# Performance work log

Hardware: AMD Instinct MI355X
Metric: run time of the kernel (lower is better)

Reference implementation:

```python
import jax, jax.numpy as jnp
import numpy as np

N, E, G = 20000, 600000, 128
NF, HID, L, H = 16, 128, 4, 4
C = HID // H  # 32 per-head out dim
BN_EPS = 1e-5


def setup_inputs() -> dict:
    key = jax.random.key(0)
    ks = jax.random.split(key, 24)
    inp = {}
    inp['x'] = jax.random.normal(ks[0], (N, NF), dtype=jnp.float32)
    inp['edge_index'] = jax.random.randint(ks[1], (2, E), 0, N, dtype=jnp.int32)
    inp['batch'] = jnp.sort(jax.random.randint(ks[2], (N,), 0, G, dtype=jnp.int32))
    s = 0.05
    inp['emb_w'] = jax.random.normal(ks[3], (NF, HID), dtype=jnp.float32) * s
    inp['emb_b'] = jnp.zeros((HID,), dtype=jnp.float32)
    inp['gat_w'] = jax.random.normal(ks[4], (L, HID, HID), dtype=jnp.float32) * s
    inp['att_src'] = jax.random.normal(ks[5], (L, H, C), dtype=jnp.float32) * s
    inp['att_dst'] = jax.random.normal(ks[6], (L, H, C), dtype=jnp.float32) * s
    inp['gat_b'] = jnp.zeros((L, HID), dtype=jnp.float32)
    inp['bn_gamma'] = jnp.ones((L, HID), dtype=jnp.float32)
    inp['bn_beta'] = jnp.zeros((L, HID), dtype=jnp.float32)
    inp['bn_mean'] = jax.random.normal(ks[7], (L, HID), dtype=jnp.float32) * 0.01
    inp['bn_var'] = jnp.ones((L, HID), dtype=jnp.float32)
    inp['fc1_w'] = jax.random.normal(ks[8], (HID, 64), dtype=jnp.float32) * s
    inp['fc1_b'] = jnp.zeros((64,), dtype=jnp.float32)
    inp['fc2_w'] = jax.random.normal(ks[9], (64, 32), dtype=jnp.float32) * s
    inp['fc2_b'] = jnp.zeros((32,), dtype=jnp.float32)
    inp['bg_w'] = jax.random.normal(ks[10], (32, 1), dtype=jnp.float32) * s
    inp['bg_b'] = jnp.zeros((1,), dtype=jnp.float32)
    return inp


def _gat_layer(x, W, a_src, a_dst, bias, src, dst):
    # PyG GATConv (concat=True, negative_slope=0.2, self-loops already appended)
    h = (x @ W).reshape(N, H, C)                      # [N,H,C]
    s_src = jnp.sum(h * a_src, axis=-1)               # [N,H]
    s_dst = jnp.sum(h * a_dst, axis=-1)               # [N,H]
    e = jax.nn.leaky_relu(s_src[src] + s_dst[dst], 0.2)  # [E+N,H]
    m = jax.ops.segment_max(e, dst, num_segments=N)   # per-dest softmax max
    ex = jnp.exp(e - m[dst])
    denom = jax.ops.segment_sum(ex, dst, num_segments=N)
    alpha = ex / (denom[dst] + 1e-16)                 # [E+N,H]
    msg = h[src] * alpha[:, :, None]                  # [E+N,H,C]
    out = jax.ops.segment_sum(msg, dst, num_segments=N)
    return out.reshape(N, HID) + bias


def reference(x, edge_index, batch, emb_w, emb_b, gat_w, att_src, att_dst, gat_b,
              bn_gamma, bn_beta, bn_mean, bn_var, fc1_w, fc1_b, fc2_w, fc2_b, bg_w, bg_b):
    # add self loops (PyG GATConv default)
    loops = jnp.arange(N, dtype=edge_index.dtype)
    src = jnp.concatenate([edge_index[0], loops])
    dst = jnp.concatenate([edge_index[1], loops])

    h = jax.nn.relu(x @ emb_w + emb_b)
    for l in range(L):
        hn = _gat_layer(h, gat_w[l], att_src[l], att_dst[l], gat_b[l], src, dst)
        hn = (hn - bn_mean[l]) * (bn_gamma[l] / jnp.sqrt(bn_var[l] + BN_EPS)) + bn_beta[l]
        h = h + jax.nn.relu(hn)

    # global mean pool over graphs
    sums = jax.ops.segment_sum(h, batch, num_segments=G)
    cnts = jax.ops.segment_sum(jnp.ones((N,), dtype=h.dtype), batch, num_segments=G)
    g = sums / jnp.maximum(cnts, 1.0)[:, None]        # [G,HID]

    g = jax.nn.relu(g @ fc1_w + fc1_b)
    g = jax.nn.relu(g @ fc2_w + fc2_b)
    out = g @ bg_w + bg_b                              # band_gap head
    return out.squeeze(-1)                             # [G]
```

## Files before the change

kernel.cpp:

```cpp
#include <hip/hip_runtime.h>
#include <math.h>

#define HID 128
#define NF  16
#define NH  4
#define HC  32
#define NLAYERS 4
#define SCAN_B 256

__global__ void k_init(int* __restrict__ counts, int N,
                       const float* __restrict__ gat_b, const float* __restrict__ gamma,
                       const float* __restrict__ beta, const float* __restrict__ mean,
                       const float* __restrict__ var,
                       float* __restrict__ scale, float* __restrict__ shift) {
    int i = blockIdx.x * blockDim.x + threadIdx.x;
    if (i < N) counts[i] = 1;
    if (i < NLAYERS * HID) {
        float sc = gamma[i] / sqrtf(var[i] + 1e-5f);
        scale[i] = sc;
        shift[i] = beta[i] + (gat_b[i] - mean[i]) * sc;
    }
}

__global__ void k_count_edges(const int* __restrict__ dst, int E, int* __restrict__ counts) {
    int i = blockIdx.x * blockDim.x + threadIdx.x;
    if (i < E) atomicAdd(&counts[dst[i]], 1);
}

__global__ __launch_bounds__(SCAN_B) void k_partial(const int* __restrict__ counts,
                                                    int* __restrict__ partials, int N) {
    __shared__ int s[SCAN_B];
    const int t = threadIdx.x;
    const int i = blockIdx.x * SCAN_B + t;
    int v = (i < N) ? counts[i] : 0;
    s[t] = v;
    __syncthreads();
#pragma unroll
    for (int off = SCAN_B / 2; off >= 1; off >>= 1) {
        if (t < off) s[t] += s[t + off];
        __syncthreads();
    }
    if (t == 0) partials[blockIdx.x] = s[0];
}

__global__ __launch_bounds__(128) void k_scanp(const int* __restrict__ partials,
                                               int* __restrict__ bases,
                                               int* __restrict__ row_ptr_N, int B) {
    __shared__ int s[128];
    const int t = threadIdx.x;
    int v = (t < B) ? partials[t] : 0;
    s[t] = v;
    __syncthreads();
    for (int off = 1; off < 128; off <<= 1) {
        int u = (t >= off) ? s[t - off] : 0;
        __syncthreads();
        s[t] += u;
        __syncthreads();
    }
    if (t < B) bases[t] = s[t] - v;
    if (t == 127) *row_ptr_N = s[127];
}

__global__ __launch_bounds__(SCAN_B) void k_final(const int* __restrict__ counts,
                                                  const int* __restrict__ bases,
                                                  int* __restrict__ row_ptr,
                                                  int* __restrict__ col,
                                                  int* __restrict__ fill, int N) {
    __shared__ int s[SCAN_B];
    const int t = threadIdx.x;
    const int i = blockIdx.x * SCAN_B + t;
    const int v = (i < N) ? counts[i] : 0;
    s[t] = v;
    __syncthreads();
    for (int off = 1; off < SCAN_B; off <<= 1) {
        int u = (t >= off) ? s[t - off] : 0;
        __syncthreads();
        s[t] += u;
        __syncthreads();
    }
    if (i < N) {
        const int row = bases[blockIdx.x] + s[t] - v;
        row_ptr[i] = row;
        col[row] = i;
        fill[i] = 1;
    }
}

__global__ void k_scatter(const int* __restrict__ src, const int* __restrict__ dst, int E,
                          const int* __restrict__ row_ptr, int* __restrict__ fill,
                          int* __restrict__ col) {
    int i = blockIdx.x * blockDim.x + threadIdx.x;
    if (i < E) {
        int d = dst[i];
        int pos = atomicAdd(&fill[d], 1);
        col[row_ptr[d] + pos] = src[i];
    }
}

__global__ __launch_bounds__(256) void k_embed(const float* __restrict__ x,
                                               const float* __restrict__ w,
                                               const float* __restrict__ b,
                                               float* __restrict__ h, int N) {
    __shared__ float ws_[NF * HID];
    __shared__ float bs[HID];
    const int t = threadIdx.x;
    for (int i = t; i < NF * HID; i += 256) ws_[i] = w[i];
    if (t < HID) bs[t] = b[t];
    __syncthreads();
    const int n = blockIdx.x * 2 + (t >> 7);
    const int j = t & 127;
    if (n >= N) return;
    float a = bs[j];
    const float4* xp = (const float4*)(x + (size_t)n * NF);
#pragma unroll
    for (int q = 0; q < 4; ++q) {
        const float4 xv = xp[q];
        a = fmaf(xv.x, ws_[(q * 4 + 0) * HID + j], a);
        a = fmaf(xv.y, ws_[(q * 4 + 1) * HID + j], a);
        a = fmaf(xv.z, ws_[(q * 4 + 2) * HID + j], a);
        a = fmaf(xv.w, ws_[(q * 4 + 3) * HID + j], a);
    }
    h[(size_t)n * HID + j] = fmaxf(a, 0.f);
}

__global__ __launch_bounds__(256) void k_gemm_attn(
    const float* __restrict__ h, const float* __restrict__ W,
    const float* __restrict__ a_src, const float* __restrict__ a_dst,
    float* __restrict__ hproj, float* __restrict__ ssrc, float* __restrict__ sdst, int N) {
    __shared__ float As[2][16][68];
    __shared__ float Bs[2][16][132];
    const int tid = threadIdx.x;
    const int m0 = blockIdx.x * 64;
    const int tx = tid & 15;
    const int ty = tid >> 4;
    float acc[4][8];
#pragma unroll
    for (int i = 0; i < 4; ++i)
#pragma unroll
        for (int j = 0; j < 8; ++j) acc[i][j] = 0.f;

    const int arow = tid >> 2;
    const int ak   = (tid & 3) << 2;
    const int brow = tid >> 4;
    const int bcol = (tid & 15) << 3;
    const int gr = m0 + arow;
    const float* aptr = h + (size_t)gr * HID + ak;
    const float* bptr = W + brow * HID + bcol;

    float4 av = (gr < N) ? *(const float4*)aptr : make_float4(0.f, 0.f, 0.f, 0.f);
    float4 bv0 = *(const float4*)bptr;
    float4 bv1 = *(const float4*)(bptr + 4);
    As[0][ak + 0][arow] = av.x; As[0][ak + 1][arow] = av.y;
    As[0][ak + 2][arow] = av.z; As[0][ak + 3][arow] = av.w;
    *(float4*)&Bs[0][brow][bcol] = bv0;
    *(float4*)&Bs[0][brow][bcol + 4] = bv1;
    __syncthreads();

    for (int k0 = 0; k0 < 8; ++k0) {
        const int cur = k0 & 1, nxt = cur ^ 1;
        if (k0 < 7) {
            av = (gr < N) ? *(const float4*)(aptr + (k0 + 1) * 16)
                          : make_float4(0.f, 0.f, 0.f, 0.f);
            bv0 = *(const float4*)(bptr + (size_t)(k0 + 1) * 16 * HID);
            bv1 = *(const float4*)(bptr + (size_t)(k0 + 1) * 16 * HID + 4);
        }
#pragma unroll
        for (int k = 0; k < 16; ++k) {
            const float4 a  = *(const float4*)&As[cur][k][ty << 2];
            const float4 b0 = *(const float4*)&Bs[cur][k][tx << 3];
            const float4 b1 = *(const float4*)&Bs[cur][k][(tx << 3) + 4];
            const float aa[4] = {a.x, a.y, a.z, a.w};
            const float bb[8] = {b0.x, b0.y, b0.z, b0.w, b1.x, b1.y, b1.z, b1.w};
#pragma unroll
            for (int i = 0; i < 4; ++i)
#pragma unroll
                for (int j = 0; j < 8; ++j) acc[i][j] = fmaf(aa[i], bb[j], acc[i][j]);
        }
        if (k0 < 7) {
            As[nxt][ak + 0][arow] = av.x; As[nxt][ak + 1][arow] = av.y;
            As[nxt][ak + 2][arow] = av.z; As[nxt][ak + 3][arow] = av.w;
            *(float4*)&Bs[nxt][brow][bcol] = bv0;
            *(float4*)&Bs[nxt][brow][bcol + 4] = bv1;
        }
        __syncthreads();
    }

    const int head = tx >> 2;
    float asv[8], adv[8];
#pragma unroll
    for (int j = 0; j < 8; ++j) {
        asv[j] = a_src[head * HC + (tx & 3) * 8 + j];
        adv[j] = a_dst[head * HC + (tx & 3) * 8 + j];
    }
#pragma unroll
    for (int i = 0; i < 4; ++i) {
        const int r = m0 + (ty << 2) + i;
        if (r < N) {
            const float4 o0 = make_float4(acc[i][0], acc[i][1], acc[i][2], acc[i][3]);
            const float4 o1 = make_float4(acc[i][4], acc[i][5], acc[i][6], acc[i][7]);
            *(float4*)(hproj + (size_t)r * HID + (tx << 3)) = o0;
            *(float4*)(hproj + (size_t)r * HID + (tx << 3) + 4) = o1;
            float ps = 0.f, pd = 0.f;
#pragma unroll
            for (int j = 0; j < 8; ++j) {
                ps = fmaf(acc[i][j], asv[j], ps);
                pd = fmaf(acc[i][j], adv[j], pd);
            }
            ps += __shfl_xor(ps, 1); ps += __shfl_xor(ps, 2);
            pd += __shfl_xor(pd, 1); pd += __shfl_xor(pd, 2);
            if ((tx & 3) == 0) { ssrc[r * NH + head] = ps; sdst[r * NH + head] = pd; }
        }
    }
}

#define LEAKY(e) ((e) > 0.f ? (e) : 0.2f * (e))
__global__ __launch_bounds__(256) void k_sagg(
    float* __restrict__ h, const float4* __restrict__ hproj4,
    const float4* __restrict__ ssrc4, const float4* __restrict__ sdst4,
    const int* __restrict__ row_ptr, const int* __restrict__ col,
    const float4* __restrict__ scale4, const float4* __restrict__ shift4, int N) {
    __shared__ int   s_col[4][64];
    __shared__ float s_alpha[4][256];
    const int t = threadIdx.x;
    const int w = t >> 6;
    const int lane = t & 63;
    const int n = blockIdx.x * 4 + w;
    if (n >= N) return;
    const int beg = row_ptr[n], end = row_ptr[n + 1];
    const float4 sd = sdst4[n];

    const int i0 = beg + lane;
    const bool v0 = i0 < end;
    int sn0 = 0;
    float fe0 = -1e30f, fe1 = -1e30f, fe2 = -1e30f, fe3 = -1e30f;
    float M0 = -1e30f, M1 = -1e30f, M2 = -1e30f, M3 = -1e30f;
    if (v0) {
        sn0 = col[i0];
        const float4 ss = ssrc4[sn0];
        fe0 = LEAKY(ss.x + sd.x); fe1 = LEAKY(ss.y + sd.y);
        fe2 = LEAKY(ss.z + sd.z); fe3 = LEAKY(ss.w + sd.w);
        M0 = fe0; M1 = fe1; M2 = fe2; M3 = fe3;
    }
    for (int i = i0 + 64; i < end; i += 64) {
        const float4 ss = ssrc4[col[i]];
        M0 = fmaxf(M0, LEAKY(ss.x + sd.x));
        M1 = fmaxf(M1, LEAKY(ss.y + sd.y));
        M2 = fmaxf(M2, LEAKY(ss.z + sd.z));
        M3 = fmaxf(M3, LEAKY(ss.w + sd.w));
    }
#pragma unroll
    for (int o = 32; o >= 1; o >>= 1) {
        M0 = fmaxf(M0, __shfl_xor(M0, o));
        M1 = fmaxf(M1, __shfl_xor(M1, o));
        M2 = fmaxf(M2, __shfl_xor(M2, o));
        M3 = fmaxf(M3, __shfl_xor(M3, o));
    }
    float S0 = 0.f, S1 = 0.f, S2 = 0.f, S3 = 0.f;
    float t0 = 0.f, t1 = 0.f, t2 = 0.f, t3 = 0.f;
    if (v0) {
        t0 = __expf(fe0 - M0); t1 = __expf(fe1 - M1);
        t2 = __expf(fe2 - M2); t3 = __expf(fe3 - M3);
        S0 = t0; S1 = t1; S2 = t2; S3 = t3;
    }
    for (int i = i0 + 64; i < end; i += 64) {
        const float4 ss = ssrc4[col[i]];
        S0 += __expf(LEAKY(ss.x + sd.x) - M0);
        S1 += __expf(LEAKY(ss.y + sd.y) - M1);
        S2 += __expf(LEAKY(ss.z + sd.z) - M2);
        S3 += __expf(LEAKY(ss.w + sd.w) - M3);
    }
#pragma unroll
    for (int o = 32; o >= 1; o >>= 1) {
        S0 += __shfl_xor(S0, o);
        S1 += __shfl_xor(S1, o);
        S2 += __shfl_xor(S2, o);
        S3 += __shfl_xor(S3, o);
    }
    const float inv0 = 1.f / (S0 + 1e-16f);
    const float inv1 = 1.f / (S1 + 1e-16f);
    const float inv2 = 1.f / (S2 + 1e-16f);
    const float inv3 = 1.f / (S3 + 1e-16f);

    const int c  = lane & 31;
    const int hh = c >> 3;
    const int eh = lane >> 5;
    float4 acc = make_float4(0.f, 0.f, 0.f, 0.f);
    {
        if (v0) {
            s_col[w][lane] = sn0;
            float4 a;
            a.x = t0 * inv0; a.y = t1 * inv1; a.z = t2 * inv2; a.w = t3 * inv3;
            *(float4*)&s_alpha[w][lane << 2] = a;
        }
        asm volatile("s_waitcnt lgkmcnt(0)" ::: "memory");
        const int cnt = min(64, end - beg);
#pragma unroll 4
        for (int j2 = 0; j2 < cnt; j2 += 2) {
            const int j = j2 + eh;
            float a = 0.f; int sn = s_col[w][0];
            if (j < cnt) { sn = s_col[w][j]; a = s_alpha[w][(j << 2) | hh]; }
            const float4 hv = hproj4[(size_t)sn * 32 + c];
            acc.x = fmaf(a, hv.x, acc.x);
            acc.y = fmaf(a, hv.y, acc.y);
            acc.z = fmaf(a, hv.z, acc.z);
            acc.w = fmaf(a, hv.w, acc.w);
        }
    }
    for (int c0 = beg + 64; c0 < end; c0 += 64) {
        const int i = c0 + lane;
        if (i < end) {
            const int sn = col[i];
            const float4 ss = ssrc4[sn];
            float4 a;
            a.x = __expf(LEAKY(ss.x + sd.x) - M0) * inv0;
            a.y = __expf(LEAKY(ss.y + sd.y) - M1) * inv1;
            a.z = __expf(LEAKY(ss.z + sd.z) - M2) * inv2;
            a.w = __expf(LEAKY(ss.w + sd.w) - M3) * inv3;
            s_col[w][lane] = sn;
            *(float4*)&s_alpha[w][lane << 2] = a;
        }
        asm volatile("s_waitcnt lgkmcnt(0)" ::: "memory");
        const int cnt = min(64, end - c0);
#pragma unroll 4
        for (int j2 = 0; j2 < cnt; j2 += 2) {
            const int j = j2 + eh;
            float a = 0.f; int sn = s_col[w][0];
            if (j < cnt) { sn = s_col[w][j]; a = s_alpha[w][(j << 2) | hh]; }
            const float4 hv = hproj4[(size_t)sn * 32 + c];
            acc.x = fmaf(a, hv.x, acc.x);
            acc.y = fmaf(a, hv.y, acc.y);
            acc.z = fmaf(a, hv.z, acc.z);
            acc.w = fmaf(a, hv.w, acc.w);
        }
    }
    acc.x += __shfl_xor(acc.x, 32);
    acc.y += __shfl_xor(acc.y, 32);
    acc.z += __shfl_xor(acc.z, 32);
    acc.w += __shfl_xor(acc.w, 32);

    if (lane < 32) {
        const float4 sc = scale4[c];
        const float4 sh = shift4[c];
        float4* hp = (float4*)h + (size_t)n * 32 + c;
        float4 hv = *hp;
        hv.x += fmaxf(fmaf(acc.x, sc.x, sh.x), 0.f);
        hv.y += fmaxf(fmaf(acc.y, sc.y, sh.y), 0.f);
        hv.z += fmaxf(fmaf(acc.z, sc.z, sh.z), 0.f);
        hv.w += fmaxf(fmaf(acc.w, sc.w, sh.w), 0.f);
        *hp = hv;
    }
}

__global__ __launch_bounds__(256) void k_poolhead(
    const float4* __restrict__ h4, const int* __restrict__ batch,
    const float* __restrict__ w1, const float* __restrict__ b1,
    const float* __restrict__ w2, const float* __restrict__ b2,
    const float* __restrict__ w3, const float* __restrict__ b3,
    float* __restrict__ out, int N) {
    __shared__ float4 red[8][32];
    __shared__ float gp[HID];
    __shared__ float l1[64];
    __shared__ float l2[32];
    const int g = blockIdx.x;
    const int t = threadIdx.x;
    const int c4 = t & 31, r = t >> 5;
    int lo = 0, hi = N;
    while (lo < hi) { int mid = (lo + hi) >> 1; if (batch[mid] < g) lo = mid + 1; else hi = mid; }
    int lo2 = lo, hi2 = N;
    while (lo2 < hi2) { int mid = (lo2 + hi2) >> 1; if (batch[mid] < g + 1) lo2 = mid + 1; else hi2 = mid; }
    float4 acc = make_float4(0.f, 0.f, 0.f, 0.f);
    for (int i = lo + r; i < lo2; i += 8) {
        const float4 v = h4[(size_t)i * 32 + c4];
        acc.x += v.x; acc.y += v.y; acc.z += v.z; acc.w += v.w;
    }
    red[r][c4] = acc;
    __syncthreads();
    if (r == 0) {
#pragma unroll
        for (int k = 1; k < 8; ++k) {
            const float4 v = red[k][c4];
            acc.x += v.x; acc.y += v.y; acc.z += v.z; acc.w += v.w;
        }
        const float invc = 1.f / fmaxf((float)(lo2 - lo), 1.f);
        float4 o = make_float4(acc.x * invc, acc.y * invc, acc.z * invc, acc.w * invc);
        *(float4*)&gp[c4 << 2] = o;
    }
    __syncthreads();
    if (t < 64) {
        float a = b1[t];
        for (int k = 0; k < HID; ++k) a = fmaf(gp[k], w1[k * 64 + t], a);
        l1[t] = fmaxf(a, 0.f);
    }
    __syncthreads();
    if (t < 32) {
        float a2 = b2[t];
        for (int k = 0; k < 64; ++k) a2 = fmaf(l1[k], w2[k * 32 + t], a2);
        l2[t] = fmaxf(a2, 0.f);
    }
    __syncthreads();
    if (t == 0) {
        float a3 = b3[0];
        for (int k = 0; k < 32; ++k) a3 = fmaf(l2[k], w3[k], a3);
        out[g] = a3;
    }
}

extern "C" void kernel_launch(void* const* d_in, const int* in_sizes, int n_in,
                              void* d_out, int out_size, void* d_ws, size_t ws_size,
                              hipStream_t stream) {
    const float* x        = (const float*)d_in[0];
    const int*   eidx     = (const int*)d_in[1];
    const int*   batch    = (const int*)d_in[2];
    const float* emb_w    = (const float*)d_in[3];
    const float* emb_b    = (const float*)d_in[4];
    const float* gat_w    = (const float*)d_in[5];
    const float* att_src  = (const float*)d_in[6];
    const float* att_dst  = (const float*)d_in[7];
    const float* gat_b    = (const float*)d_in[8];
    const float* bn_gamma = (const float*)d_in[9];
    const float* bn_beta  = (const float*)d_in[10];
    const float* bn_mean  = (const float*)d_in[11];
    const float* bn_var   = (const float*)d_in[12];
    const float* fc1_w    = (const float*)d_in[13];
    const float* fc1_b    = (const float*)d_in[14];
    const float* fc2_w    = (const float*)d_in[15];
    const float* fc2_b    = (const float*)d_in[16];
    const float* bg_w     = (const float*)d_in[17];
    const float* bg_b     = (const float*)d_in[18];
    float* out = (float*)d_out;

    const int N = in_sizes[0] / NF;
    const int E = in_sizes[1] / 2;
    const int G = out_size;

    const int* esrc = eidx;
    const int* edst = eidx + E;

    char* ws = (char*)d_ws;
    size_t off = 0;
    auto alloc = [&](size_t bytes) -> void* {
        void* p = ws + off;
        off += (bytes + 255) & ~(size_t)255;
        return p;
    };
    float*  h        = (float*)alloc((size_t)N * HID * sizeof(float));
    float*  hproj    = (float*)alloc((size_t)N * HID * sizeof(float));
    float*  ssrc     = (float*)alloc((size_t)N * NH * sizeof(float));
    float*  sdst     = (float*)alloc((size_t)N * NH * sizeof(float));
    float*  bnscale  = (float*)alloc((size_t)NLAYERS * HID * sizeof(float));
    float*  bnshift  = (float*)alloc((size_t)NLAYERS * HID * sizeof(float));
    int*    row_ptr  = (int*)alloc((size_t)(N + 1) * sizeof(int));
    int*    counts   = (int*)alloc((size_t)N * sizeof(int));
    int*    col      = (int*)alloc((size_t)(E + N) * sizeof(int));
    int*    partials = (int*)alloc(1024 * sizeof(int));
    int*    bases    = (int*)alloc(1024 * sizeof(int));
    (void)ws_size; (void)n_in;

    const int TB = 256;
    const int NB = (N + SCAN_B - 1) / SCAN_B;

    k_init<<<(N + TB - 1) / TB, TB, 0, stream>>>(counts, N, gat_b, bn_gamma, bn_beta,
                                                 bn_mean, bn_var, bnscale, bnshift);
    k_count_edges<<<(E + TB - 1) / TB, TB, 0, stream>>>(edst, E, counts);
    k_partial<<<NB, SCAN_B, 0, stream>>>(counts, partials, N);
    k_scanp<<<1, 128, 0, stream>>>(partials, bases, row_ptr + N, NB);
    k_final<<<NB, SCAN_B, 0, stream>>>(counts, bases, row_ptr, col, counts, N);
    k_scatter<<<(E + TB - 1) / TB, TB, 0, stream>>>(esrc, edst, E, row_ptr, counts, col);

    k_embed<<<(N + 1) / 2, 256, 0, stream>>>(x, emb_w, emb_b, h, N);

    for (int l = 0; l < NLAYERS; ++l) {
        k_gemm_attn<<<(N + 63) / 64, 256, 0, stream>>>(
            h, gat_w + (size_t)l * HID * HID,
            att_src + (size_t)l * NH * HC, att_dst + (size_t)l * NH * HC,
            hproj, ssrc, sdst, N);
        k_sagg<<<(N + 3) / 4, 256, 0, stream>>>(
            h, (const float4*)hproj, (const float4*)ssrc, (const float4*)sdst,
            row_ptr, col,
            (const float4*)(bnscale + l * HID), (const float4*)(bnshift + l * HID), N);
    }

    k_poolhead<<<G, 256, 0, stream>>>((const float4*)h, batch,
                                      fc1_w, fc1_b, fc2_w, fc2_b, bg_w, bg_b, out, N);
}
```

Before: 354.7 us.

## Process each destination node with a two-wave block in GAT aggregation

Restructures the softmax-aggregation kernel so each node is handled by a 128-thread block of two wavefronts instead of one wavefront per node. The max and sum reductions and the final accumulator reduction now go across both waves through shared memory and block barriers. The edge window grows to 128, and four edge slots are processed in parallel per feature column. With an average degree around 31, most lanes sit idle, and the extra __syncthreads add overhead, so the added parallelism per node may not pay off.

```diff
diff --git a/kernel.cpp b/kernel.cpp
--- a/kernel.cpp
+++ b/kernel.cpp
@@ -214,22 +214,24 @@
 }
 
 #define LEAKY(e) ((e) > 0.f ? (e) : 0.2f * (e))
-__global__ __launch_bounds__(256) void k_sagg(
+__global__ __launch_bounds__(128) void k_sagg(
     float* __restrict__ h, const float4* __restrict__ hproj4,
     const float4* __restrict__ ssrc4, const float4* __restrict__ sdst4,
     const int* __restrict__ row_ptr, const int* __restrict__ col,
     const float4* __restrict__ scale4, const float4* __restrict__ shift4, int N) {
-    __shared__ int   s_col[4][64];
-    __shared__ float s_alpha[4][256];
-    const int t = threadIdx.x;
-    const int w = t >> 6;
-    const int lane = t & 63;
-    const int n = blockIdx.x * 4 + w;
-    if (n >= N) return;
+    __shared__ int    s_col[128];
+    __shared__ float  s_alpha[128 * 4];
+    __shared__ float4 s_ms[2];
+    __shared__ float4 s_red[32];
+    const int tid = threadIdx.x;
+    const int wv  = tid >> 6;
+    const int lane = tid & 63;
+    const int n = blockIdx.x;
     const int beg = row_ptr[n], end = row_ptr[n + 1];
+    const int deg = end - beg;
     const float4 sd = sdst4[n];
 
-    const int i0 = beg + lane;
+    const int i0 = beg + tid;
     const bool v0 = i0 < end;
     int sn0 = 0;
     float fe0 = -1e30f, fe1 = -1e30f, fe2 = -1e30f, fe3 = -1e30f;
@@ -241,7 +243,7 @@
         fe2 = LEAKY(ss.z + sd.z); fe3 = LEAKY(ss.w + sd.w);
         M0 = fe0; M1 = fe1; M2 = fe2; M3 = fe3;
     }
-    for (int i = i0 + 64; i < end; i += 64) {
+    for (int i = i0 + 128; i < end; i += 128) {
         const float4 ss = ssrc4[col[i]];
         M0 = fmaxf(M0, LEAKY(ss.x + sd.x));
         M1 = fmaxf(M1, LEAKY(ss.y + sd.y));
@@ -255,14 +257,23 @@
         M2 = fmaxf(M2, __shfl_xor(M2, o));
         M3 = fmaxf(M3, __shfl_xor(M3, o));
     }
+    if (lane == 0) s_ms[wv] = make_float4(M0, M1, M2, M3);
+    __syncthreads();
+    {
+        const float4 mo = s_ms[wv ^ 1];
+        M0 = fmaxf(M0, mo.x); M1 = fmaxf(M1, mo.y);
+        M2 = fmaxf(M2, mo.z); M3 = fmaxf(M3, mo.w);
+    }
+    __syncthreads();
+
+    float t0 = 0.f, t1 = 0.f, t2 = 0.f, t3 = 0.f;
     float S0 = 0.f, S1 = 0.f, S2 = 0.f, S3 = 0.f;
-    float t0 = 0.f, t1 = 0.f, t2 = 0.f, t3 = 0.f;
     if (v0) {
         t0 = __expf(fe0 - M0); t1 = __expf(fe1 - M1);
         t2 = __expf(fe2 - M2); t3 = __expf(fe3 - M3);
         S0 = t0; S1 = t1; S2 = t2; S3 = t3;
     }
-    for (int i = i0 + 64; i < end; i += 64) {
+    for (int i = i0 + 128; i < end; i += 128) {
         const float4 ss = ssrc4[col[i]];
         S0 += __expf(LEAKY(ss.x + sd.x) - M0);
         S1 += __expf(LEAKY(ss.y + sd.y) - M1);
@@ -276,29 +287,36 @@
         S2 += __shfl_xor(S2, o);
         S3 += __shfl_xor(S3, o);
     }
+    if (lane == 0) s_ms[wv] = make_float4(S0, S1, S2, S3);
+    __syncthreads();
+    {
+        const float4 so = s_ms[wv ^ 1];
+        S0 += so.x; S1 += so.y; S2 += so.z; S3 += so.w;
+    }
     const float inv0 = 1.f / (S0 + 1e-16f);
     const float inv1 = 1.f / (S1 + 1e-16f);
     const float inv2 = 1.f / (S2 + 1e-16f);
     const float inv3 = 1.f / (S3 + 1e-16f);
 
-    const int c  = lane & 31;
-    const int hh = c >> 3;
-    const int eh = lane >> 5;
+    if (v0) {
+        s_col[tid] = sn0;
+        float4 a;
+        a.x = t0 * inv0; a.y = t1 * inv1; a.z = t2 * inv2; a.w = t3 * inv3;
+        *(float4*)&s_alpha[tid << 2] = a;
+    }
+    __syncthreads();
+
+    const int c    = lane & 31;
+    const int hh   = c >> 3;
+    const int slot = (wv << 1) | (lane >> 5);
     float4 acc = make_float4(0.f, 0.f, 0.f, 0.f);
     {
-        if (v0) {
-            s_col[w][lane] = sn0;
-            float4 a;
-            a.x = t0 * inv0; a.y = t1 * inv1; a.z = t2 * inv2; a.w = t3 * inv3;
-            *(float4*)&s_alpha[w][lane << 2] = a;
-        }
-        asm volatile("s_waitcnt lgkmcnt(0)" ::: "memory");
-        const int cnt = min(64, end - beg);
+        const int cnt = min(128, deg);
 #pragma unroll 4
-        for (int j2 = 0; j2 < cnt; j2 += 2) {
-            const int j = j2 + eh;
-            float a = 0.f; int sn = s_col[w][0];
-            if (j < cnt) { sn = s_col[w][j]; a = s_alpha[w][(j << 2) | hh]; }
+        for (int j4 = 0; j4 < cnt; j4 += 4) {
+            const int j = j4 + slot;
+            float a = 0.f; int sn = s_col[0];
+            if (j < cnt) { sn = s_col[j]; a = s_alpha[(j << 2) | hh]; }
             const float4 hv = hproj4[(size_t)sn * 32 + c];
             acc.x = fmaf(a, hv.x, acc.x);
             acc.y = fmaf(a, hv.y, acc.y);
@@ -306,8 +324,9 @@
             acc.w = fmaf(a, hv.w, acc.w);
         }
     }
-    for (int c0 = beg + 64; c0 < end; c0 += 64) {
-        const int i = c0 + lane;
+    for (int c0 = beg + 128; c0 < end; c0 += 128) {
+        __syncthreads();
+        const int i = c0 + tid;
         if (i < end) {
             const int sn = col[i];
             const float4 ss = ssrc4[sn];
@@ -316,16 +335,16 @@
             a.y = __expf(LEAKY(ss.y + sd.y) - M1) * inv1;
             a.z = __expf(LEAKY(ss.z + sd.z) - M2) * inv2;
             a.w = __expf(LEAKY(ss.w + sd.w) - M3) * inv3;
-            s_col[w][lane] = sn;
-            *(float4*)&s_alpha[w][lane << 2] = a;
-        }
-        asm volatile("s_waitcnt lgkmcnt(0)" ::: "memory");
-        const int cnt = min(64, end - c0);
+            s_col[tid] = sn;
+            *(float4*)&s_alpha[tid << 2] = a;
+        }
+        __syncthreads();
+        const int cnt = min(128, end - c0);
 #pragma unroll 4
-        for (int j2 = 0; j2 < cnt; j2 += 2) {
-            const int j = j2 + eh;
-            float a = 0.f; int sn = s_col[w][0];
-            if (j < cnt) { sn = s_col[w][j]; a = s_alpha[w][(j << 2) | hh]; }
+        for (int j4 = 0; j4 < cnt; j4 += 4) {
+            const int j = j4 + slot;
+            float a = 0.f; int sn = s_col[0];
+            if (j < cnt) { sn = s_col[j]; a = s_alpha[(j << 2) | hh]; }
             const float4 hv = hproj4[(size_t)sn * 32 + c];
             acc.x = fmaf(a, hv.x, acc.x);
             acc.y = fmaf(a, hv.y, acc.y);
@@ -337,8 +356,11 @@
     acc.y += __shfl_xor(acc.y, 32);
     acc.z += __shfl_xor(acc.z, 32);
     acc.w += __shfl_xor(acc.w, 32);
-
-    if (lane < 32) {
+    if (wv == 1 && lane < 32) s_red[c] = acc;
+    __syncthreads();
+    if (wv == 0 && lane < 32) {
+        const float4 r = s_red[c];
+        acc.x += r.x; acc.y += r.y; acc.z += r.z; acc.w += r.w;
         const float4 sc = scale4[c];
         const float4 sh = shift4[c];
         float4* hp = (float4*)h + (size_t)n * 32 + c;
@@ -474,7 +496,7 @@
             h, gat_w + (size_t)l * HID * HID,
             att_src + (size_t)l * NH * HC, att_dst + (size_t)l * NH * HC,
             hproj, ssrc, sdst, N);
-        k_sagg<<<(N + 3) / 4, 256, 0, stream>>>(
+        k_sagg<<<N, 128, 0, stream>>>(
             h, (const float4*)hproj, (const float4*)ssrc, (const float4*)sdst,
             row_ptr, col,
             (const float4*)(bnscale + l * HID), (const float4*)(bnshift + l * HID), N);
```

Measured after the change: 364.6 us. +2.8%, slower.
